# Kernel tuning notes

Measured on AMD Instinct MI355X. Metric: run time of the kernel, lower is better.

Reference implementation:

```python
import jax, jax.numpy as jnp
import numpy as np

N = 100000   # nodes
E = 1600000  # edges
F = 128      # num_features
H = 128      # embedding_size
C = 10       # num_classes
G = 64       # graphs in batch


def setup_inputs() -> dict:
    key = jax.random.key(0)
    ks = jax.random.split(key, 10)
    x = jax.random.normal(ks[0], (N, F), jnp.float32)
    edge_index = jax.random.randint(ks[1], (2, E), 0, N)
    batch_index = jnp.sort(jax.random.randint(ks[2], (N,), 0, G))
    glorot = lambda k, shape: jax.random.normal(k, shape, jnp.float32) / np.float32(np.sqrt(shape[0]))
    return {
        "x": x, "edge_index": edge_index, "batch_index": batch_index,
        "W0": glorot(ks[3], (F, H)), "b0": jnp.zeros((H,), jnp.float32),
        "W1": glorot(ks[4], (H, H)), "b1": jnp.zeros((H,), jnp.float32),
        "W2": glorot(ks[5], (H, H)), "b2": jnp.zeros((H,), jnp.float32),
        "W3": glorot(ks[6], (H, H)), "b3": jnp.zeros((H,), jnp.float32),
        "Wout": glorot(ks[7], (2 * H, C)), "bout": jnp.zeros((C,), jnp.float32),
    }


def gcn_conv(x, W, b, src, dst):
    """PyG GCNConv: self-loops + symmetric D^-1/2 (A+I) D^-1/2 normalization."""
    n = x.shape[0]
    # degree with self-loop: deg[i] = 1 + in-degree(i)
    deg = 1.0 + jax.ops.segment_sum(jnp.ones(dst.shape[0], x.dtype), dst, num_segments=n)
    dinv = jax.lax.rsqrt(deg)
    h = x @ W  # [N, H]
    norm = (dinv[src] * dinv[dst])[:, None]  # [E, 1]
    agg = jax.ops.segment_sum(h[src] * norm, dst, num_segments=n)  # scatter-add over edges
    agg = agg + h * (1.0 / deg)[:, None]  # self-loop contribution dinv[i]^2 * h[i]
    return agg + b


def reference(x, edge_index, batch_index, W0, b0, W1, b1, W2, b2, W3, b3, Wout, bout):
    src, dst = edge_index[0], edge_index[1]
    h = jnp.tanh(gcn_conv(x, W0, b0, src, dst))
    h = jnp.tanh(gcn_conv(h, W1, b1, src, dst))
    h = jnp.tanh(gcn_conv(h, W2, b2, src, dst))
    h = jnp.tanh(gcn_conv(h, W3, b3, src, dst))
    # global max pool + global mean pool over batch_index
    gmax = jax.ops.segment_max(h, batch_index, num_segments=G)
    cnt = jax.ops.segment_sum(jnp.ones((h.shape[0],), h.dtype), batch_index, num_segments=G)
    gmean = jax.ops.segment_sum(h, batch_index, num_segments=G) / jnp.maximum(cnt, 1.0)[:, None]
    pooled = jnp.concatenate([gmax, gmean], axis=1)  # [G, 2H]
    out = pooled @ Wout + bout  # [G, C]
    return out, pooled
```

## Files before the change

kernel.cpp:

```cpp
#include <hip/hip_runtime.h>
#include <hip/hip_fp16.h>
#include <cmath>

typedef __attribute__((ext_vector_type(8))) short short8;
typedef __attribute__((ext_vector_type(8))) unsigned short ushort8;
typedef __attribute__((ext_vector_type(4))) float f32x4;

struct h8 { __half2 a, b, c, d; };

__device__ __forceinline__ unsigned pk_bf16(float a, float b) {
  unsigned r;
  asm("v_cvt_pk_bf16_f32 %0, %1, %2" : "=v"(r) : "v"(a), "v"(b));
  return r;
}

__device__ __forceinline__ float fast_tanh(float x) {
  float e2 = __expf(2.0f * x);
  return 1.0f - 2.0f * __builtin_amdgcn_rcpf(e2 + 1.0f);
}


__global__ __launch_bounds__(256) void count_k(const int* __restrict__ dst,
                                               int* __restrict__ cnt,
                                               int* __restrict__ epos, int E) {
  int e = blockIdx.x * 256 + threadIdx.x;
  if (e < E) epos[e] = atomicAdd(&cnt[dst[e]], 1);
}

__global__ __launch_bounds__(512) void scan_a(const int* __restrict__ cnt,
                                              int* __restrict__ rs,
                                              int* __restrict__ bsum,
                                              float* __restrict__ dinv,
                                              float* __restrict__ dinv2, int n) {
  __shared__ int s[512];
  int tid = threadIdx.x;
  int gid = blockIdx.x * 512 + tid;
  int v = (gid < n) ? cnt[gid] : 0;
  if (gid < n) {
    float deg = 1.0f + (float)v;
    dinv[gid] = rsqrtf(deg);
    dinv2[gid] = __builtin_amdgcn_rcpf(deg);
  }
  s[tid] = v;
  __syncthreads();
  for (int off = 1; off < 512; off <<= 1) {
    int t = (tid >= off) ? s[tid - off] : 0;
    __syncthreads();
    s[tid] += t;
    __syncthreads();
  }
  if (gid < n) rs[gid] = s[tid] - v;
  if (tid == 511) bsum[blockIdx.x] = s[511];
}

__global__ __launch_bounds__(256) void scan_b(const int* __restrict__ bsum,
                                              int* __restrict__ boff, int nb,
                                              const int* __restrict__ batch,
                                              int* __restrict__ gstart, int n,
                                              int G) {
  __shared__ int s[256];
  int tid = threadIdx.x;
  int v = (tid < nb) ? bsum[tid] : 0;
  s[tid] = v;
  __syncthreads();
  for (int off = 1; off < 256; off <<= 1) {
    int t = (tid >= off) ? s[tid - off] : 0;
    __syncthreads();
    s[tid] += t;
    __syncthreads();
  }
  if (tid < nb) boff[tid] = s[tid] - v;
  if (tid <= G) {
    int lo = 0, hi = n;
    while (lo < hi) {
      int mid = (lo + hi) >> 1;
      if (batch[mid] < tid) lo = mid + 1;
      else hi = mid;
    }
    gstart[tid] = lo;
  }
}

__global__ __launch_bounds__(512) void scan_c(const int* __restrict__ boff,
                                              int* __restrict__ rs, int n, int E) {
  int gid = blockIdx.x * 512 + threadIdx.x;
  if (gid < n) rs[gid] += boff[blockIdx.x];
  if (gid == 0) rs[n] = E;
}

__global__ __launch_bounds__(256) void fill_k(const int* __restrict__ src,
                                              const int* __restrict__ dst,
                                              const int* __restrict__ rs,
                                              const int* __restrict__ epos,
                                              const float* __restrict__ dinv,
                                              int* __restrict__ col,
                                              float* __restrict__ normv, int E) {
  int e = blockIdx.x * 256 + threadIdx.x;
  if (e >= E) return;
  int s = src[e], d = dst[e];
  int pos = rs[d] + epos[e];
  col[pos] = s;
  normv[pos] = dinv[s] * dinv[d];
}


__global__ __launch_bounds__(256) void wconv_all(const float* __restrict__ W0,
                                                 const float* __restrict__ W1,
                                                 const float* __restrict__ W2,
                                                 const float* __restrict__ W3,
                                                 unsigned short* __restrict__ WtHi,
                                                 unsigned short* __restrict__ WtLo) {
  int l = blockIdx.y;
  const float* W = (l == 0) ? W0 : (l == 1) ? W1 : (l == 2) ? W2 : W3;
  int idx = blockIdx.x * 256 + threadIdx.x;
  if (idx >= 8192) return;
  int n = idx & 127, k = (idx >> 7) * 2;
  float w0 = W[k * 128 + n], w1 = W[(k + 1) * 128 + n];
  unsigned h01 = pk_bf16(w0, w1);
  float hf0 = __uint_as_float(h01 << 16);
  float hf1 = __uint_as_float(h01 & 0xFFFF0000u);
  unsigned l01 = pk_bf16(w0 - hf0, w1 - hf1);
  *(unsigned*)&WtHi[l * 16384 + n * 128 + k] = h01;
  *(unsigned*)&WtLo[l * 16384 + n * 128 + k] = l01;
}


#define LDK 136

__global__ __launch_bounds__(256) void gemm_mfma(const float* __restrict__ A,
                                                 const unsigned short* __restrict__ WtHi,
                                                 const unsigned short* __restrict__ WtLo,
                                                 __half* __restrict__ O, int M) {
  __shared__ unsigned short sHi[128 * LDK];
  __shared__ unsigned short sLo[128 * LDK];
  int tid = threadIdx.x;
#pragma unroll
  for (int i = 0; i < 8; ++i) {
    int c = tid + i * 256;
    int n = c >> 4;
    int off = (c & 15) * 8;
    *(ushort8*)&sHi[n * LDK + off] = *(const ushort8*)&WtHi[c * 8];
    *(ushort8*)&sLo[n * LDK + off] = *(const ushort8*)&WtLo[c * 8];
  }
  __syncthreads();

  int wv = tid >> 6, lane = tid & 63;
  int r0 = blockIdx.x * 128 + wv * 32;
  int lrow = lane & 15, lk = (lane >> 4) * 8;

  f32x4 acc[2][8] = {};
#pragma unroll
  for (int kk = 0; kk < 4; ++kk) {
    int k0 = kk * 32 + lk;
    short8 ahi[2], alo[2];
#pragma unroll
    for (int fr = 0; fr < 2; ++fr) {
      int row = r0 + fr * 16 + lrow;
      row = row < M ? row : M - 1;
      const float* ap = &A[(size_t)row * 128 + k0];
      float4 a0 = *(const float4*)ap;
      float4 a1 = *(const float4*)(ap + 4);
      union { short8 v; unsigned u32[4]; } h_, l_;
#define SPLIT2(slot, x, y)                              \
      {                                                 \
        unsigned hh = pk_bf16((x), (y));                \
        h_.u32[slot] = hh;                              \
        float hf0 = __uint_as_float(hh << 16);          \
        float hf1 = __uint_as_float(hh & 0xFFFF0000u);  \
        l_.u32[slot] = pk_bf16((x) - hf0, (y) - hf1);   \
      }
      SPLIT2(0, a0.x, a0.y)
      SPLIT2(1, a0.z, a0.w)
      SPLIT2(2, a1.x, a1.y)
      SPLIT2(3, a1.z, a1.w)
#undef SPLIT2
      ahi[fr] = h_.v;
      alo[fr] = l_.v;
    }
#pragma unroll
    for (int c = 0; c < 8; ++c) {
      int bidx = (c * 16 + lrow) * LDK + k0;
      short8 bhi = *(const short8*)&sHi[bidx];
      short8 blo = *(const short8*)&sLo[bidx];
#pragma unroll
      for (int fr = 0; fr < 2; ++fr) {
        acc[fr][c] = __builtin_amdgcn_mfma_f32_16x16x32_bf16(ahi[fr], bhi, acc[fr][c], 0, 0, 0);
        acc[fr][c] = __builtin_amdgcn_mfma_f32_16x16x32_bf16(ahi[fr], blo, acc[fr][c], 0, 0, 0);
        acc[fr][c] = __builtin_amdgcn_mfma_f32_16x16x32_bf16(alo[fr], bhi, acc[fr][c], 0, 0, 0);
      }
    }
  }
#pragma unroll
  for (int fr = 0; fr < 2; ++fr) {
#pragma unroll
    for (int c = 0; c < 8; ++c) {
#pragma unroll
      for (int r = 0; r < 4; ++r) {
        int row = r0 + fr * 16 + (lane >> 4) * 4 + r;
        if (row < M)
          O[(size_t)row * 128 + c * 16 + (lane & 15)] = __float2half(acc[fr][c][r]);
      }
    }
  }
}


__global__ __launch_bounds__(256) void gather_k(const __half* __restrict__ h,
                                                const int* __restrict__ rs,
                                                const int* __restrict__ col,
                                                const float* __restrict__ normv,
                                                const float* __restrict__ dinv2,
                                                const float* __restrict__ bias,
                                                float* __restrict__ out, int N) {
  int wid = (int)((blockIdx.x * (size_t)blockDim.x + threadIdx.x) >> 6);
  if (wid >= N) return;
  int lane = threadIdx.x & 63;
  int grp = lane >> 4;
  int li = lane & 15;
  int s = rs[wid], e = rs[wid + 1];
  const h8* hrow = (const h8*)h;

  float ac[8] = {};
  int n16 = (e - s) >> 4;
  int base = s + grp;
  for (int it = 0; it < n16; ++it, base += 16) {
    int c0 = col[base], c1 = col[base + 4], c2 = col[base + 8], c3 = col[base + 12];
    float w0 = normv[base], w1 = normv[base + 4], w2 = normv[base + 8],
          w3 = normv[base + 12];
    h8 v0 = hrow[(size_t)c0 * 16 + li];
    h8 v1 = hrow[(size_t)c1 * 16 + li];
    h8 v2 = hrow[(size_t)c2 * 16 + li];
    h8 v3 = hrow[(size_t)c3 * 16 + li];
#define ACC(V, W)                                    \
    {                                                \
      float2 f0 = __half22float2((V).a);             \
      float2 f1 = __half22float2((V).b);             \
      float2 f2 = __half22float2((V).c);             \
      float2 f3 = __half22float2((V).d);             \
      ac[0] += (W) * f0.x; ac[1] += (W) * f0.y;      \
      ac[2] += (W) * f1.x; ac[3] += (W) * f1.y;      \
      ac[4] += (W) * f2.x; ac[5] += (W) * f2.y;      \
      ac[6] += (W) * f3.x; ac[7] += (W) * f3.y;      \
    }
    ACC(v0, w0) ACC(v1, w1) ACC(v2, w2) ACC(v3, w3)
  }
  for (int idx = base; idx < e; idx += 4) {
    int c = col[idx];
    float w = normv[idx];
    h8 v = hrow[(size_t)c * 16 + li];
    ACC(v, w)
  }
#undef ACC
#pragma unroll
  for (int j = 0; j < 8; ++j) {
    ac[j] += __shfl_xor(ac[j], 16);
    ac[j] += __shfl_xor(ac[j], 32);
  }

  float a0 = grp == 0 ? ac[0] : grp == 1 ? ac[2] : grp == 2 ? ac[4] : ac[6];
  float a1 = grp == 0 ? ac[1] : grp == 1 ? ac[3] : grp == 2 ? ac[5] : ac[7];

  float d2 = dinv2[wid];
  h8 sv = hrow[(size_t)wid * 16 + li];
  __half2 svh = grp == 0 ? sv.a : grp == 1 ? sv.b : grp == 2 ? sv.c : sv.d;
  float2 sj = __half22float2(svh);
  float2 bj = *(const float2*)&bias[li * 8 + 2 * grp];
  float o0 = fast_tanh(a0 + sj.x * d2 + bj.x);
  float o1 = fast_tanh(a1 + sj.y * d2 + bj.y);
  *(float2*)&out[(size_t)wid * 128 + li * 8 + 2 * grp] = make_float2(o0, o1);
}


#define CH 16

__global__ __launch_bounds__(128) void pool_partial(const float* __restrict__ h,
                                                    const int* __restrict__ gstart,
                                                    float* __restrict__ pmax,
                                                    float* __restrict__ psum) {
  int g = blockIdx.x, c = blockIdx.y, f = threadIdx.x;
  int s = gstart[g], e = gstart[g + 1];
  long long len = e - s;
  int cs = s + (int)(len * c / CH);
  int ce = s + (int)(len * (c + 1) / CH);
  float m = -INFINITY, sum = 0.f;
  for (int n = cs; n < ce; ++n) {
    float v = h[(size_t)n * 128 + f];
    m = fmaxf(m, v);
    sum += v;
  }
  pmax[((size_t)g * CH + c) * 128 + f] = m;
  psum[((size_t)g * CH + c) * 128 + f] = sum;
}

__global__ __launch_bounds__(128) void pool_head(const float* __restrict__ pmax,
                                                 const float* __restrict__ psum,
                                                 const int* __restrict__ gstart,
                                                 const float* __restrict__ Wout,
                                                 const float* __restrict__ bout,
                                                 float* __restrict__ out, int G) {
  __shared__ float pl[256];
  int g = blockIdx.x, f = threadIdx.x;
  float m = -INFINITY, s = 0.f;
  for (int c = 0; c < CH; ++c) {
    m = fmaxf(m, pmax[((size_t)g * CH + c) * 128 + f]);
    s += psum[((size_t)g * CH + c) * 128 + f];
  }
  int cnt = gstart[g + 1] - gstart[g];
  float mean = s / fmaxf((float)cnt, 1.0f);
  float* pooled = out + (size_t)G * 10;
  pooled[(size_t)g * 256 + f] = m;
  pooled[(size_t)g * 256 + 128 + f] = mean;
  pl[f] = m;
  pl[128 + f] = mean;
  __syncthreads();
  if (f < 10) {
    float acc = bout[f];
    for (int k = 0; k < 256; ++k) acc += pl[k] * Wout[k * 10 + f];
    out[(size_t)g * 10 + f] = acc;
  }
}


extern "C" void kernel_launch(void* const* d_in, const int* in_sizes, int n_in,
                              void* d_out, int out_size, void* d_ws, size_t ws_size,
                              hipStream_t stream) {
  const float* x = (const float*)d_in[0];
  const int* ei = (const int*)d_in[1];
  const int* batch = (const int*)d_in[2];
  const float* W[4] = {(const float*)d_in[3], (const float*)d_in[5],
                       (const float*)d_in[7], (const float*)d_in[9]};
  const float* Bz[4] = {(const float*)d_in[4], (const float*)d_in[6],
                        (const float*)d_in[8], (const float*)d_in[10]};
  const float* Wout = (const float*)d_in[11];
  const float* bout = (const float*)d_in[12];
  const int N = in_sizes[0] / 128;
  const int E = in_sizes[1] / 2;
  const int G = 64;
  const int* srcp = ei;
  const int* dstp = ei + E;
  float* out = (float*)d_out;

  char* wsb = (char*)d_ws;
  size_t off = 0;
  auto alloc = [&](size_t bytes) -> void* {
    void* p = wsb + off;
    off = (off + bytes + 255) & ~(size_t)255;
    return p;
  };
  __half* bufA = (__half*)alloc((size_t)N * 128 * 2);
  float* bufB = (float*)alloc((size_t)N * 128 * 4);
  int* cnt = (int*)alloc((size_t)N * 4);
  int* epos = (int*)alloc((size_t)E * 4);
  float* dinv = (float*)alloc((size_t)N * 4);
  float* dinv2 = (float*)alloc((size_t)N * 4);
  int* rs = (int*)alloc((size_t)(N + 1) * 4);
  int* col = (int*)alloc((size_t)E * 4);
  float* normv = (float*)alloc((size_t)E * 4);
  int* bsum = (int*)alloc(4096);
  int* boff = (int*)alloc(4096);
  int* gstart = (int*)alloc(4096);
  float* pmax = (float*)alloc((size_t)G * CH * 128 * 4);
  float* psum = (float*)alloc((size_t)G * CH * 128 * 4);
  unsigned short* WtHi = (unsigned short*)alloc(4 * 16384 * 2);
  unsigned short* WtLo = (unsigned short*)alloc(4 * 16384 * 2);
  if (off > ws_size) return;

  hipMemsetAsync(cnt, 0, (size_t)N * 4, stream);

  count_k<<<(E + 255) / 256, 256, 0, stream>>>(dstp, cnt, epos, E);
  int nsb = (N + 511) / 512;
  scan_a<<<nsb, 512, 0, stream>>>(cnt, rs, bsum, dinv, dinv2, N);
  scan_b<<<1, 256, 0, stream>>>(bsum, boff, nsb, batch, gstart, N, G);
  scan_c<<<nsb, 512, 0, stream>>>(boff, rs, N, E);
  fill_k<<<(E + 255) / 256, 256, 0, stream>>>(srcp, dstp, rs, epos, dinv, col,
                                              normv, E);
  wconv_all<<<dim3(32, 4), 256, 0, stream>>>(W[0], W[1], W[2], W[3], WtHi, WtLo);

  const float* in = x;
  for (int l = 0; l < 4; ++l) {
    gemm_mfma<<<(N + 127) / 128, 256, 0, stream>>>(in, WtHi + l * 16384,
                                                   WtLo + l * 16384, bufA, N);
    gather_k<<<((size_t)N * 64 + 255) / 256, 256, 0, stream>>>(bufA, rs, col, normv,
                                                               dinv2, Bz[l], bufB, N);
    in = bufB;
  }

  pool_partial<<<dim3(G, CH), 128, 0, stream>>>(bufB, gstart, pmax, psum);
  pool_head<<<G, 128, 0, stream>>>(pmax, psum, gstart, Wout, bout, out, G);
}
```

Measured before the change: 541.3 us.

## Emit bf16 hi/lo split from gather and interleave edge col/norm

The gather kernel now writes its tanh output directly as packed bf16 hi and lo halves, so layers 1-3 use a new GEMM that loads pre-split A operands instead of converting fp32 at load time. Pooling reads the two bf16 planes and recombines them. Edge column indices and normalization weights are also packed into a single int2 array, so each edge takes one 8-byte load. This removes the fp32 split work inside the GEMM and one separate load per edge, at the cost of a small precision change in the stored activations.

```diff
diff --git a/kernel.cpp b/kernel.cpp
--- a/kernel.cpp
+++ b/kernel.cpp
@@ -93,14 +93,15 @@
                                               const int* __restrict__ rs,
                                               const int* __restrict__ epos,
                                               const float* __restrict__ dinv,
-                                              int* __restrict__ col,
-                                              float* __restrict__ normv, int E) {
+                                              int2* __restrict__ edata, int E) {
   int e = blockIdx.x * 256 + threadIdx.x;
   if (e >= E) return;
   int s = src[e], d = dst[e];
   int pos = rs[d] + epos[e];
-  col[pos] = s;
-  normv[pos] = dinv[s] * dinv[d];
+  int2 ed;
+  ed.x = s;
+  ed.y = __float_as_int(dinv[s] * dinv[d]);
+  edata[pos] = ed;
 }
 
 
@@ -204,14 +205,75 @@
   }
 }
 
+__global__ __launch_bounds__(256) void gemm_fast(const unsigned short* __restrict__ AHi,
+                                                 const unsigned short* __restrict__ ALo,
+                                                 const unsigned short* __restrict__ WtHi,
+                                                 const unsigned short* __restrict__ WtLo,
+                                                 __half* __restrict__ O, int M) {
+  __shared__ unsigned short sHi[128 * LDK];
+  __shared__ unsigned short sLo[128 * LDK];
+  int tid = threadIdx.x;
+#pragma unroll
+  for (int i = 0; i < 8; ++i) {
+    int c = tid + i * 256;
+    int n = c >> 4;
+    int off = (c & 15) * 8;
+    *(ushort8*)&sHi[n * LDK + off] = *(const ushort8*)&WtHi[c * 8];
+    *(ushort8*)&sLo[n * LDK + off] = *(const ushort8*)&WtLo[c * 8];
+  }
+  __syncthreads();
+
+  int wv = tid >> 6, lane = tid & 63;
+  int r0 = blockIdx.x * 128 + wv * 32;
+  int lrow = lane & 15, lk = (lane >> 4) * 8;
+
+  f32x4 acc[2][8] = {};
+#pragma unroll
+  for (int kk = 0; kk < 4; ++kk) {
+    int k0 = kk * 32 + lk;
+    short8 ahi[2], alo[2];
+#pragma unroll
+    for (int fr = 0; fr < 2; ++fr) {
+      int row = r0 + fr * 16 + lrow;
+      row = row < M ? row : M - 1;
+      ahi[fr] = *(const short8*)&AHi[(size_t)row * 128 + k0];
+      alo[fr] = *(const short8*)&ALo[(size_t)row * 128 + k0];
+    }
+#pragma unroll
+    for (int c = 0; c < 8; ++c) {
+      int bidx = (c * 16 + lrow) * LDK + k0;
+      short8 bhi = *(const short8*)&sHi[bidx];
+      short8 blo = *(const short8*)&sLo[bidx];
+#pragma unroll
+      for (int fr = 0; fr < 2; ++fr) {
+        acc[fr][c] = __builtin_amdgcn_mfma_f32_16x16x32_bf16(ahi[fr], bhi, acc[fr][c], 0, 0, 0);
+        acc[fr][c] = __builtin_amdgcn_mfma_f32_16x16x32_bf16(ahi[fr], blo, acc[fr][c], 0, 0, 0);
+        acc[fr][c] = __builtin_amdgcn_mfma_f32_16x16x32_bf16(alo[fr], bhi, acc[fr][c], 0, 0, 0);
+      }
+    }
+  }
+#pragma unroll
+  for (int fr = 0; fr < 2; ++fr) {
+#pragma unroll
+    for (int c = 0; c < 8; ++c) {
+#pragma unroll
+      for (int r = 0; r < 4; ++r) {
+        int row = r0 + fr * 16 + (lane >> 4) * 4 + r;
+        if (row < M)
+          O[(size_t)row * 128 + c * 16 + (lane & 15)] = __float2half(acc[fr][c][r]);
+      }
+    }
+  }
+}
+
 
 __global__ __launch_bounds__(256) void gather_k(const __half* __restrict__ h,
                                                 const int* __restrict__ rs,
-                                                const int* __restrict__ col,
-                                                const float* __restrict__ normv,
+                                                const int2* __restrict__ edata,
                                                 const float* __restrict__ dinv2,
                                                 const float* __restrict__ bias,
-                                                float* __restrict__ out, int N) {
+                                                unsigned* __restrict__ OHi,
+                                                unsigned* __restrict__ OLo, int N) {
   int wid = (int)((blockIdx.x * (size_t)blockDim.x + threadIdx.x) >> 6);
   if (wid >= N) return;
   int lane = threadIdx.x & 63;
@@ -224,13 +286,14 @@
   int n16 = (e - s) >> 4;
   int base = s + grp;
   for (int it = 0; it < n16; ++it, base += 16) {
-    int c0 = col[base], c1 = col[base + 4], c2 = col[base + 8], c3 = col[base + 12];
-    float w0 = normv[base], w1 = normv[base + 4], w2 = normv[base + 8],
-          w3 = normv[base + 12];
-    h8 v0 = hrow[(size_t)c0 * 16 + li];
-    h8 v1 = hrow[(size_t)c1 * 16 + li];
-    h8 v2 = hrow[(size_t)c2 * 16 + li];
-    h8 v3 = hrow[(size_t)c3 * 16 + li];
+    int2 e0 = edata[base], e1 = edata[base + 4], e2 = edata[base + 8],
+         e3 = edata[base + 12];
+    float w0 = __int_as_float(e0.y), w1 = __int_as_float(e1.y),
+          w2 = __int_as_float(e2.y), w3 = __int_as_float(e3.y);
+    h8 v0 = hrow[(size_t)e0.x * 16 + li];
+    h8 v1 = hrow[(size_t)e1.x * 16 + li];
+    h8 v2 = hrow[(size_t)e2.x * 16 + li];
+    h8 v3 = hrow[(size_t)e3.x * 16 + li];
 #define ACC(V, W)                                    \
     {                                                \
       float2 f0 = __half22float2((V).a);             \
@@ -245,9 +308,9 @@
     ACC(v0, w0) ACC(v1, w1) ACC(v2, w2) ACC(v3, w3)
   }
   for (int idx = base; idx < e; idx += 4) {
-    int c = col[idx];
-    float w = normv[idx];
-    h8 v = hrow[(size_t)c * 16 + li];
+    int2 ed = edata[idx];
+    float w = __int_as_float(ed.y);
+    h8 v = hrow[(size_t)ed.x * 16 + li];
     ACC(v, w)
   }
 #undef ACC
@@ -267,13 +330,21 @@
   float2 bj = *(const float2*)&bias[li * 8 + 2 * grp];
   float o0 = fast_tanh(a0 + sj.x * d2 + bj.x);
   float o1 = fast_tanh(a1 + sj.y * d2 + bj.y);
-  *(float2*)&out[(size_t)wid * 128 + li * 8 + 2 * grp] = make_float2(o0, o1);
+
+  unsigned hp = pk_bf16(o0, o1);
+  float r0f = __uint_as_float(hp << 16);
+  float r1f = __uint_as_float(hp & 0xFFFF0000u);
+  unsigned lp = pk_bf16(o0 - r0f, o1 - r1f);
+  unsigned idx = (unsigned)wid * 64 + li * 4 + grp;
+  OHi[idx] = hp;
+  OLo[idx] = lp;
 }
 
 
 #define CH 16
 
-__global__ __launch_bounds__(128) void pool_partial(const float* __restrict__ h,
+__global__ __launch_bounds__(128) void pool_partial(const unsigned short* __restrict__ Hi,
+                                                    const unsigned short* __restrict__ Lo,
                                                     const int* __restrict__ gstart,
                                                     float* __restrict__ pmax,
                                                     float* __restrict__ psum) {
@@ -284,7 +355,9 @@
   int ce = s + (int)(len * (c + 1) / CH);
   float m = -INFINITY, sum = 0.f;
   for (int n = cs; n < ce; ++n) {
-    float v = h[(size_t)n * 128 + f];
+    unsigned hv = Hi[(size_t)n * 128 + f];
+    unsigned lv = Lo[(size_t)n * 128 + f];
+    float v = __uint_as_float(hv << 16) + __uint_as_float(lv << 16);
     m = fmaxf(m, v);
     sum += v;
   }
@@ -348,14 +421,14 @@
     return p;
   };
   __half* bufA = (__half*)alloc((size_t)N * 128 * 2);
-  float* bufB = (float*)alloc((size_t)N * 128 * 4);
+  unsigned* OHi = (unsigned*)alloc((size_t)N * 64 * 4);
+  unsigned* OLo = (unsigned*)alloc((size_t)N * 64 * 4);
   int* cnt = (int*)alloc((size_t)N * 4);
   int* epos = (int*)alloc((size_t)E * 4);
   float* dinv = (float*)alloc((size_t)N * 4);
   float* dinv2 = (float*)alloc((size_t)N * 4);
   int* rs = (int*)alloc((size_t)(N + 1) * 4);
-  int* col = (int*)alloc((size_t)E * 4);
-  float* normv = (float*)alloc((size_t)E * 4);
+  int2* edata = (int2*)alloc((size_t)E * 8);
   int* bsum = (int*)alloc(4096);
   int* boff = (int*)alloc(4096);
   int* gstart = (int*)alloc(4096);
@@ -372,19 +445,24 @@
   scan_a<<<nsb, 512, 0, stream>>>(cnt, rs, bsum, dinv, dinv2, N);
   scan_b<<<1, 256, 0, stream>>>(bsum, boff, nsb, batch, gstart, N, G);
   scan_c<<<nsb, 512, 0, stream>>>(boff, rs, N, E);
-  fill_k<<<(E + 255) / 256, 256, 0, stream>>>(srcp, dstp, rs, epos, dinv, col,
-                                              normv, E);
+  fill_k<<<(E + 255) / 256, 256, 0, stream>>>(srcp, dstp, rs, epos, dinv, edata, E);
   wconv_all<<<dim3(32, 4), 256, 0, stream>>>(W[0], W[1], W[2], W[3], WtHi, WtLo);
 
-  const float* in = x;
   for (int l = 0; l < 4; ++l) {
-    gemm_mfma<<<(N + 127) / 128, 256, 0, stream>>>(in, WtHi + l * 16384,
-                                                   WtLo + l * 16384, bufA, N);
-    gather_k<<<((size_t)N * 64 + 255) / 256, 256, 0, stream>>>(bufA, rs, col, normv,
-                                                               dinv2, Bz[l], bufB, N);
-    in = bufB;
-  }
-
-  pool_partial<<<dim3(G, CH), 128, 0, stream>>>(bufB, gstart, pmax, psum);
+    if (l == 0)
+      gemm_mfma<<<(N + 127) / 128, 256, 0, stream>>>(x, WtHi, WtLo, bufA, N);
+    else
+      gemm_fast<<<(N + 127) / 128, 256, 0, stream>>>((const unsigned short*)OHi,
+                                                     (const unsigned short*)OLo,
+                                                     WtHi + l * 16384,
+                                                     WtLo + l * 16384, bufA, N);
+    gather_k<<<((size_t)N * 64 + 255) / 256, 256, 0, stream>>>(bufA, rs, edata,
+                                                               dinv2, Bz[l], OHi,
+                                                               OLo, N);
+  }
+
+  pool_partial<<<dim3(G, CH), 128, 0, stream>>>((const unsigned short*)OHi,
+                                                (const unsigned short*)OLo, gstart,
+                                                pmax, psum);
   pool_head<<<G, 128, 0, stream>>>(pmax, psum, gstart, Wout, bout, out, G);
 }
```

After: 537.2 us. No clear change (-0.8%).
